# Kernel optimization log

Measured on AMD Instinct MI355X. Metric: run time of the kernel, lower is better.

## Reference

```python
import jax, jax.numpy as jnp
import numpy as np

EMBED_DIM = 1024
NUM_HEADS = 16
HEAD_DIM = EMBED_DIM // NUM_HEADS


def setup_inputs() -> dict:
    key = jax.random.key(0)
    kq, kk, kv, kw1, kw2 = jax.random.split(key, 5)
    B, S, D = 4, 2048, EMBED_DIM
    # xavier_uniform with gain=0.1
    lim_qkv = 0.1 * np.sqrt(6.0 / (D + 3 * D))
    lim_out = 0.1 * np.sqrt(6.0 / (D + D))
    return {
        "query": jax.random.normal(kq, (B, S, D), dtype=jnp.float32),
        "key": jax.random.normal(kk, (B, S, D), dtype=jnp.float32),
        "value": jax.random.normal(kv, (B, S, D), dtype=jnp.float32),
        "W_qkv": jax.random.uniform(kw1, (3 * D, D), jnp.float32, -lim_qkv, lim_qkv),
        "b_qkv": jnp.zeros((3 * D,), jnp.float32),
        "W_out": jax.random.uniform(kw2, (D, D), jnp.float32, -lim_out, lim_out),
        "b_out": jnp.zeros((D,), jnp.float32),
    }


def reference(query, key, value, W_qkv, b_qkv, W_out, b_out):
    # NOTE: the torch module computes Q,K,V all from `query` (self-attention);
    # `key`/`value` args are API placeholders and unused in the math.
    B, S, D = query.shape
    qkv = query @ W_qkv.T + b_qkv                     # [B,S,3D]
    qkv = qkv.reshape(B, S, 3, NUM_HEADS, HEAD_DIM)
    q = qkv[:, :, 0].transpose(0, 2, 1, 3)            # [B,H,S,hd]
    k = qkv[:, :, 1].transpose(0, 2, 1, 3)
    v = qkv[:, :, 2].transpose(0, 2, 1, 3)
    scale = 1.0 / np.sqrt(HEAD_DIM)
    scores = jnp.einsum("bhqd,bhkd->bhqk", q, k) * scale
    attn = jax.nn.softmax(scores, axis=-1)
    out = jnp.einsum("bhqk,bhkd->bhqd", attn, v)      # [B,H,S,hd]
    out = out.transpose(0, 2, 1, 3).reshape(B, S, D)
    return out @ W_out.T + b_out
```

## Files before the change

### kernel.cpp

```cpp
#include <hip/hip_runtime.h>

typedef __attribute__((ext_vector_type(8))) __bf16 bf16x8;
typedef __attribute__((ext_vector_type(4))) float f32x4;
typedef unsigned short u16;
typedef unsigned int u32;

__device__ __forceinline__ u16 f2bf(float x) {
  u32 u = __builtin_bit_cast(u32, x);
  u = (u + 0x7FFFu + ((u >> 16) & 1u)) >> 16;
  return (u16)u;
}

#define BAR()                          \
  {                                    \
    asm volatile("" ::: "memory");     \
    __builtin_amdgcn_s_barrier();      \
    asm volatile("" ::: "memory");     \
  }

__global__ __launch_bounds__(256) void cvt_f32_bf16(
    const float* __restrict__ in, u16* __restrict__ out, int n8) {
  int i = blockIdx.x * 256 + threadIdx.x;
  if (i >= n8) return;
  const float4* p = reinterpret_cast<const float4*>(in) + (size_t)i * 2;
  float4 a = p[0], b = p[1];
  uint4 r;
  r.x = (u32)f2bf(a.x) | ((u32)f2bf(a.y) << 16);
  r.y = (u32)f2bf(a.z) | ((u32)f2bf(a.w) << 16);
  r.z = (u32)f2bf(b.x) | ((u32)f2bf(b.y) << 16);
  r.w = (u32)f2bf(b.z) | ((u32)f2bf(b.w) << 16);
  reinterpret_cast<uint4*>(out)[i] = r;
}

__global__ __launch_bounds__(512, 2) void gemm_qkv8(
    const u16* __restrict__ A, const u16* __restrict__ Bw,
    const float* __restrict__ bias, u16* __restrict__ Qh,
    u16* __restrict__ Kh, u16* __restrict__ Vt) {
  constexpr int K = 1024;
  constexpr int NT = 16;
  __shared__ u16 Als[2][2][128][64];
  __shared__ u16 Bls[2][2][128][64];
  u16* const ALp = &Als[0][0][0][0];
  u16* const BLp = &Bls[0][0][0][0];

  const int tid = threadIdx.x;
  const int w = tid >> 6, l = tid & 63;
  const int kg = l >> 4, lr = l & 15;
  const int wr = w >> 2, wc = w & 3;
  const int bid = blockIdx.x;
  const int wg = (bid & 7) * 48 + (bid >> 3);
  const int tm = wg / 12, tn = wg % 12;

  const int r0 = tid >> 3, c0 = tid & 7;
  const int lc0 = c0 ^ (r0 & 7);
  const int ldsOff0 = tid * 8, ldsOff1 = tid * 8 + 4096;
  const u16* aSrc0[2];
  const u16* bSrc0[2];
#pragma unroll
  for (int h = 0; h < 2; ++h) {
    aSrc0[h] = A + (size_t)(tm * 256 + h * 128 + r0) * K + lc0 * 8;
    bSrc0[h] = Bw + (size_t)(tn * 256 + h * 128 + r0) * K + lc0 * 8;
  }
  const size_t rowStep = (size_t)64 * K;

#define ISSUE_A(BUF, H, T)                                                      \
  {                                                                             \
    __builtin_amdgcn_global_load_lds(                                           \
        (const __attribute__((address_space(1))) void*)(aSrc0[H] + (T) * 64),   \
        (__attribute__((address_space(3))) void*)(ALp + (BUF) * 16384 +         \
                                                 (H) * 8192 + ldsOff0),         \
        16, 0, 0);                                                              \
    __builtin_amdgcn_global_load_lds(                                           \
        (const __attribute__((address_space(1))) void*)(aSrc0[H] + rowStep +    \
                                                        (T) * 64),              \
        (__attribute__((address_space(3))) void*)(ALp + (BUF) * 16384 +         \
                                                 (H) * 8192 + ldsOff1),         \
        16, 0, 0);                                                              \
  }
#define ISSUE_B(BUF, H, T)                                                      \
  {                                                                             \
    __builtin_amdgcn_global_load_lds(                                           \
        (const __attribute__((address_space(1))) void*)(bSrc0[H] + (T) * 64),   \
        (__attribute__((address_space(3))) void*)(BLp + (BUF) * 16384 +         \
                                                 (H) * 8192 + ldsOff0),         \
        16, 0, 0);                                                              \
    __builtin_amdgcn_global_load_lds(                                           \
        (const __attribute__((address_space(1))) void*)(bSrc0[H] + rowStep +    \
                                                        (T) * 64),              \
        (__attribute__((address_space(3))) void*)(BLp + (BUF) * 16384 +         \
                                                 (H) * 8192 + ldsOff1),         \
        16, 0, 0);                                                              \
  }

  const int x7 = lr & 7;
  const int pc0 = (kg ^ x7) * 8;
  const int pc1 = ((kg + 4) ^ x7) * 8;
  const int wr16lr = wr * 16 + lr;
  const int wc16lr = wc * 16 + lr;

  const f32x4 fz = {0.f, 0.f, 0.f, 0.f};
  f32x4 acc[8][4];
#pragma unroll
  for (int m = 0; m < 8; ++m)
#pragma unroll
    for (int n = 0; n < 4; ++n) acc[m][n] = fz;

  bf16x8 aF[4][2], bF[2][2];

#define READ_A(P, MH)                                                           \
  {                                                                             \
    const u16* bp = ALp + (P) * 16384 + (MH) * 8192;                            \
    _Pragma("unroll") for (int mi = 0; mi < 4; ++mi) {                          \
      const u16* rp = bp + (mi * 32 + wr16lr) * 64;                             \
      aF[mi][0] = *(const bf16x8*)(rp + pc0);                                   \
      aF[mi][1] = *(const bf16x8*)(rp + pc1);                                   \
    }                                                                           \
  }
#define READ_B(P, NH)                                                           \
  {                                                                             \
    const u16* bp = BLp + (P) * 16384 + (NH) * 8192;                            \
    _Pragma("unroll") for (int ni = 0; ni < 2; ++ni) {                          \
      const u16* rp = bp + (ni * 64 + wc16lr) * 64;                             \
      bF[ni][0] = *(const bf16x8*)(rp + pc0);                                   \
      bF[ni][1] = *(const bf16x8*)(rp + pc1);                                   \
    }                                                                           \
  }
#define MFMA_Q(MH, NH)                                                          \
  {                                                                             \
    _Pragma("unroll") for (int mi = 0; mi < 4; ++mi)                            \
        _Pragma("unroll") for (int ni = 0; ni < 2; ++ni) {                      \
      acc[(MH)*4 + mi][(NH)*2 + ni] = __builtin_amdgcn_mfma_f32_16x16x32_bf16(  \
          aF[mi][0], bF[ni][0], acc[(MH)*4 + mi][(NH)*2 + ni], 0, 0, 0);        \
      acc[(MH)*4 + mi][(NH)*2 + ni] = __builtin_amdgcn_mfma_f32_16x16x32_bf16(  \
          aF[mi][1], bF[ni][1], acc[(MH)*4 + mi][(NH)*2 + ni], 0, 0, 0);        \
    }                                                                           \
  }

  ISSUE_A(0, 0, 0);
  ISSUE_A(0, 1, 0);
  ISSUE_B(0, 0, 0);
  ISSUE_B(0, 1, 0);
  ISSUE_A(1, 0, 1);
  ISSUE_B(1, 1, 1);

  for (int t = 0; t < NT; ++t) {
    const int p = t & 1;
    if (t == NT - 1) {
      asm volatile("s_waitcnt vmcnt(0)" ::: "memory");
    } else {
      asm volatile("s_waitcnt vmcnt(4)" ::: "memory");
    }
    BAR();
    if (t + 1 < NT) ISSUE_B(p ^ 1, 0, t + 1);
    READ_A(p, 0);
    READ_B(p, 0);
    BAR();
    __builtin_amdgcn_s_setprio(1);
    MFMA_Q(0, 0);
    __builtin_amdgcn_s_setprio(0);
    BAR();
    if (t + 1 < NT) ISSUE_A(p ^ 1, 1, t + 1);
    READ_B(p, 1);
    BAR();
    __builtin_amdgcn_s_setprio(1);
    MFMA_Q(0, 1);
    __builtin_amdgcn_s_setprio(0);
    BAR();
    if (t + 2 < NT) ISSUE_A(p, 0, t + 2);
    READ_A(p, 1);
    BAR();
    __builtin_amdgcn_s_setprio(1);
    MFMA_Q(1, 1);
    __builtin_amdgcn_s_setprio(0);
    BAR();
    if (t + 2 < NT) ISSUE_B(p, 1, t + 2);
    READ_B(p, 0);
    BAR();
    __builtin_amdgcn_s_setprio(1);
    MFMA_Q(1, 0);
    __builtin_amdgcn_s_setprio(0);
    BAR();
  }

#pragma unroll
  for (int m = 0; m < 8; ++m) {
    const int i0 = tm * 256 + m * 32 + wr * 16 + kg * 4;
    const int b = i0 >> 11, s0 = i0 & 2047;
#pragma unroll
    for (int n = 0; n < 4; ++n) {
      const int jc = tn * 256 + n * 64 + wc * 16 + lr;
      const float bs = bias[jc];
      const int sel = jc >> 10, hh = (jc >> 6) & 15, d = jc & 63;
      if (sel == 0) {
        u16* qp = Qh + ((size_t)((b * 16 + hh) * 2048 + s0)) * 64 + d;
#pragma unroll
        for (int j = 0; j < 4; ++j)
          qp[(size_t)j * 64] = f2bf((acc[m][n][j] + bs) * 0.18033688f);
      } else if (sel == 1) {
        u16* kp = Kh + ((size_t)((b * 16 + hh) * 2048 + s0)) * 64 + d;
#pragma unroll
        for (int j = 0; j < 4; ++j) kp[(size_t)j * 64] = f2bf(acc[m][n][j] + bs);
      } else {
        ushort4 vv;
        vv.x = f2bf(acc[m][n][0] + bs);
        vv.y = f2bf(acc[m][n][1] + bs);
        vv.z = f2bf(acc[m][n][2] + bs);
        vv.w = f2bf(acc[m][n][3] + bs);
        *(ushort4*)(Vt + ((size_t)((b * 16 + hh) * 64 + d)) * 2048 + s0) = vv;
      }
    }
  }
#undef ISSUE_A
#undef ISSUE_B
#undef READ_A
#undef READ_B
#undef MFMA_Q
}

__global__ __launch_bounds__(256) void gemm_out_k(
    const u16* __restrict__ A, const u16* __restrict__ Bw,
    const float* __restrict__ bias, float* __restrict__ Cout) {
  constexpr int N = 1024, K = 1024;
  __shared__ u16 As[128 * 32];
  __shared__ u16 Bs[128 * 32];
  const int tid = threadIdx.x;
  const int w = tid >> 6, l = tid & 63;
  const int kg = l >> 4, lr = l & 15;
  const int bid = blockIdx.x;
  const int wg = (bid & 7) * 64 + (bid >> 3);
  const int tm = wg >> 3, tn = wg & 7;
  const int wr = w >> 1, wc = w & 1;

  const u16* Ab = A + (size_t)tm * 128 * K;
  const u16* Bb = Bw + (size_t)tn * 128 * K;

  const f32x4 fz = {0.f, 0.f, 0.f, 0.f};
  f32x4 acc[4][4];
#pragma unroll
  for (int m = 0; m < 4; ++m)
#pragma unroll
    for (int n = 0; n < 4; ++n) acc[m][n] = fz;

  for (int k0 = 0; k0 < K; k0 += 32) {
#pragma unroll
    for (int u = 0; u < 2; ++u) {
      int e = u * 256 + tid;
      const u16* ga = Ab + (size_t)(e >> 2) * K + k0 + (e & 3) * 8;
      const u16* gb = Bb + (size_t)(e >> 2) * K + k0 + (e & 3) * 8;
      __builtin_amdgcn_global_load_lds(
          (const __attribute__((address_space(1))) void*)ga,
          (__attribute__((address_space(3))) void*)(As + (u * 256 + w * 64) * 8),
          16, 0, 0);
      __builtin_amdgcn_global_load_lds(
          (const __attribute__((address_space(1))) void*)gb,
          (__attribute__((address_space(3))) void*)(Bs + (u * 256 + w * 64) * 8),
          16, 0, 0);
    }
    asm volatile("s_waitcnt vmcnt(0)" ::: "memory");
    __syncthreads();
    bf16x8 a[4], b[4];
#pragma unroll
    for (int m = 0; m < 4; ++m)
      a[m] = *(const bf16x8*)(As + (wr * 64 + m * 16 + lr) * 32 + kg * 8);
#pragma unroll
    for (int n = 0; n < 4; ++n)
      b[n] = *(const bf16x8*)(Bs + (wc * 64 + n * 16 + lr) * 32 + kg * 8);
#pragma unroll
    for (int m = 0; m < 4; ++m)
#pragma unroll
      for (int n = 0; n < 4; ++n)
        acc[m][n] =
            __builtin_amdgcn_mfma_f32_16x16x32_bf16(a[m], b[n], acc[m][n], 0, 0, 0);
    __syncthreads();
  }

#pragma unroll
  for (int m = 0; m < 4; ++m) {
    const int i0 = tm * 128 + wr * 64 + m * 16 + kg * 4;
#pragma unroll
    for (int n = 0; n < 4; ++n) {
      const int jc = tn * 128 + wc * 64 + n * 16 + lr;
      const float bs = bias[jc];
#pragma unroll
      for (int j = 0; j < 4; ++j)
        Cout[(size_t)(i0 + j) * N + jc] = acc[m][n][j] + bs;
    }
  }
}

__global__ __launch_bounds__(256, 4) void attn_kernel(
    const u16* __restrict__ Qh, const u16* __restrict__ Kh,
    const u16* __restrict__ Vt, u16* __restrict__ Aout) {
  __shared__ alignas(16) u16 Kl[2][4096];
  __shared__ alignas(16) u16 Vl[2][4096];
  const int tid = threadIdx.x;
  const int w = tid >> 6, l = tid & 63;
  const int kg = l >> 4, lq = l & 15;
  const int bid = blockIdx.x;
  const int wgi = (bid & 7) * 128 + (bid >> 3);
  const int bh = wgi >> 4, qt = wgi & 15;
  const int qbase = qt * 128 + w * 32;

  const u16* Qb = Qh + ((size_t)(bh * 2048 + qbase + lq)) * 64;
  const bf16x8 aq00 = *(const bf16x8*)(Qb + kg * 8);
  const bf16x8 aq01 = *(const bf16x8*)(Qb + 32 + kg * 8);
  const bf16x8 aq10 = *(const bf16x8*)(Qb + 16 * 64 + kg * 8);
  const bf16x8 aq11 = *(const bf16x8*)(Qb + 16 * 64 + 32 + kg * 8);

  const u16* Kb = Kh + (size_t)bh * 2048 * 64;
  const u16* Vb = Vt + (size_t)bh * 64 * 2048;

  const int r7K = 4 * (lq >> 3) + (lq & 3);
  const int rowbK = 8 * ((lq >> 2) & 1) + r7K;
  const int ckK0 = (kg ^ r7K) * 8;
  const int ckK1 = ((kg + 4) ^ r7K) * 8;
  const int r7V = lq & 7;
  const int ckV0 = (kg ^ r7V) * 8;
  const int ckV1 = ((kg + 4) ^ r7V) * 8;

  const f32x4 fz = {0.f, 0.f, 0.f, 0.f};
  f32x4 on0[4] = {fz, fz, fz, fz};
  f32x4 on1[4] = {fz, fz, fz, fz};
  float m0 = -1e30f, m1 = -1e30f, l0 = 0.f, l1 = 0.f;

#define STAGE_KV(buf, kc)                                                        \
  {                                                                              \
    {                                                                            \
      const int s_ = tid, row_ = s_ >> 3, c_ = s_ & 7;                           \
      const int sw_ = (c_ ^ (row_ & 7)) * 8;                                     \
      const int srow_ = (row_ & ~20) | ((row_ & 4) << 2) | ((row_ & 16) >> 2);   \
      __builtin_amdgcn_global_load_lds(                                          \
          (const __attribute__((address_space(1))) void*)(Kb + (size_t)((kc) + srow_) * 64 + sw_), \
          (__attribute__((address_space(3))) void*)(&Kl[buf][s_ * 8]), 16, 0, 0);\
      __builtin_amdgcn_global_load_lds(                                          \
          (const __attribute__((address_space(1))) void*)(Vb + (size_t)row_ * 2048 + (kc) + sw_),  \
          (__attribute__((address_space(3))) void*)(&Vl[buf][s_ * 8]), 16, 0, 0);\
    }                                                                            \
    {                                                                            \
      const int s_ = 256 + tid, row_ = s_ >> 3, c_ = s_ & 7;                     \
      const int sw_ = (c_ ^ (row_ & 7)) * 8;                                     \
      const int srow_ = (row_ & ~20) | ((row_ & 4) << 2) | ((row_ & 16) >> 2);   \
      __builtin_amdgcn_global_load_lds(                                          \
          (const __attribute__((address_space(1))) void*)(Kb + (size_t)((kc) + srow_) * 64 + sw_), \
          (__attribute__((address_space(3))) void*)(&Kl[buf][s_ * 8]), 16, 0, 0);\
      __builtin_amdgcn_global_load_lds(                                          \
          (const __attribute__((address_space(1))) void*)(Vb + (size_t)row_ * 2048 + (kc) + sw_),  \
          (__attribute__((address_space(3))) void*)(&Vl[buf][s_ * 8]), 16, 0, 0);\
    }                                                                            \
  }

  STAGE_KV(0, 0);
  asm volatile("s_waitcnt vmcnt(0)" ::: "memory");
  __syncthreads();

  int cur = 0;
  for (int kc = 0; kc < 2048; kc += 64) {
    if (kc + 64 < 2048) STAGE_KV(cur ^ 1, kc + 64);
    const u16* Klc = Kl[cur];
    const u16* Vlc = Vl[cur];

    f32x4 st0[4], st1[4];
    __builtin_amdgcn_s_setprio(1);
#pragma unroll
    for (int t = 0; t < 4; ++t) {
      const int ro = (rowbK + ((t >> 1) * 32 + (t & 1) * 16)) * 64;
      bf16x8 k0 = *(const bf16x8*)(Klc + ro + ckK0);
      bf16x8 k1 = *(const bf16x8*)(Klc + ro + ckK1);
      f32x4 z0 = fz, z1 = fz;
      z0 = __builtin_amdgcn_mfma_f32_16x16x32_bf16(k0, aq00, z0, 0, 0, 0);
      z0 = __builtin_amdgcn_mfma_f32_16x16x32_bf16(k1, aq01, z0, 0, 0, 0);
      z1 = __builtin_amdgcn_mfma_f32_16x16x32_bf16(k0, aq10, z1, 0, 0, 0);
      z1 = __builtin_amdgcn_mfma_f32_16x16x32_bf16(k1, aq11, z1, 0, 0, 0);
      st0[t] = z0;
      st1[t] = z1;
    }
    __builtin_amdgcn_s_setprio(0);

    float rm0 = st0[0][0], rm1 = st1[0][0];
#pragma unroll
    for (int t = 0; t < 4; ++t)
#pragma unroll
      for (int j = 0; j < 4; ++j) {
        rm0 = fmaxf(rm0, st0[t][j]);
        rm1 = fmaxf(rm1, st1[t][j]);
      }
    rm0 = fmaxf(rm0, __shfl_xor(rm0, 16));
    rm0 = fmaxf(rm0, __shfl_xor(rm0, 32));
    rm1 = fmaxf(rm1, __shfl_xor(rm1, 16));
    rm1 = fmaxf(rm1, __shfl_xor(rm1, 32));
    if (!__all(fmaxf(rm0 - m0, rm1 - m1) <= 8.f)) {
      float mn0 = fmaxf(m0, rm0), mn1 = fmaxf(m1, rm1);
      float a0 = __builtin_amdgcn_exp2f(m0 - mn0);
      float a1 = __builtin_amdgcn_exp2f(m1 - mn1);
      m0 = mn0;
      m1 = mn1;
      l0 *= a0;
      l1 *= a1;
#pragma unroll
      for (int j = 0; j < 4; ++j) {
        float aj0 = __shfl(a0, kg * 4 + j);
        float aj1 = __shfl(a1, kg * 4 + j);
#pragma unroll
        for (int n = 0; n < 4; ++n) {
          on0[n][j] *= aj0;
          on1[n][j] *= aj1;
        }
      }
    }

    bf16x8 pa00, pa01, pa10, pa11;
    {
      float rs = 0.f;
      float p[4][4];
#pragma unroll
      for (int t = 0; t < 4; ++t)
#pragma unroll
        for (int j = 0; j < 4; ++j) {
          p[t][j] = __builtin_amdgcn_exp2f(st0[t][j] - m0);
          rs += p[t][j];
        }
      rs += __shfl_xor(rs, 16);
      rs += __shfl_xor(rs, 32);
      l0 += rs;
#pragma unroll
      for (int j = 0; j < 4; ++j) {
        pa00[j] = (__bf16)p[0][j];
        pa00[4 + j] = (__bf16)p[1][j];
        pa01[j] = (__bf16)p[2][j];
        pa01[4 + j] = (__bf16)p[3][j];
      }
    }
    {
      float rs = 0.f;
      float p[4][4];
#pragma unroll
      for (int t = 0; t < 4; ++t)
#pragma unroll
        for (int j = 0; j < 4; ++j) {
          p[t][j] = __builtin_amdgcn_exp2f(st1[t][j] - m1);
          rs += p[t][j];
        }
      rs += __shfl_xor(rs, 16);
      rs += __shfl_xor(rs, 32);
      l1 += rs;
#pragma unroll
      for (int j = 0; j < 4; ++j) {
        pa10[j] = (__bf16)p[0][j];
        pa10[4 + j] = (__bf16)p[1][j];
        pa11[j] = (__bf16)p[2][j];
        pa11[4 + j] = (__bf16)p[3][j];
      }
    }

    __builtin_amdgcn_s_setprio(1);
#pragma unroll
    for (int n = 0; n < 4; ++n) {
      const int ro = (n * 16 + lq) * 64;
      bf16x8 v0 = *(const bf16x8*)(Vlc + ro + ckV0);
      bf16x8 v1 = *(const bf16x8*)(Vlc + ro + ckV1);
      on0[n] = __builtin_amdgcn_mfma_f32_16x16x32_bf16(pa00, v0, on0[n], 0, 0, 0);
      on0[n] = __builtin_amdgcn_mfma_f32_16x16x32_bf16(pa01, v1, on0[n], 0, 0, 0);
      on1[n] = __builtin_amdgcn_mfma_f32_16x16x32_bf16(pa10, v0, on1[n], 0, 0, 0);
      on1[n] = __builtin_amdgcn_mfma_f32_16x16x32_bf16(pa11, v1, on1[n], 0, 0, 0);
    }
    __builtin_amdgcn_s_setprio(0);

    asm volatile("s_waitcnt vmcnt(0)" ::: "memory");
    __syncthreads();
    cur ^= 1;
  }

  const int b = bh >> 4, h = bh & 15;
  {
    u16* Ob = Aout + (size_t)(b * 2048 + qbase + kg * 4) * 1024 + h * 64 + lq;
#pragma unroll
    for (int j = 0; j < 4; ++j) {
      float lj = __shfl(l0, kg * 4 + j);
      float inv = 1.f / lj;
#pragma unroll
      for (int n = 0; n < 4; ++n)
        Ob[(size_t)j * 1024 + n * 16] = f2bf(on0[n][j] * inv);
    }
  }
  {
    u16* Ob = Aout + (size_t)(b * 2048 + qbase + 16 + kg * 4) * 1024 + h * 64 + lq;
#pragma unroll
    for (int j = 0; j < 4; ++j) {
      float lj = __shfl(l1, kg * 4 + j);
      float inv = 1.f / lj;
#pragma unroll
      for (int n = 0; n < 4; ++n)
        Ob[(size_t)j * 1024 + n * 16] = f2bf(on1[n][j] * inv);
    }
  }
}

extern "C" void kernel_launch(void* const* d_in, const int* in_sizes, int n_in,
                              void* d_out, int out_size, void* d_ws, size_t ws_size,
                              hipStream_t stream) {
  const float* query = (const float*)d_in[0];
  const float* Wqkv = (const float*)d_in[3];
  const float* bqkv = (const float*)d_in[4];
  const float* Wout = (const float*)d_in[5];
  const float* bout = (const float*)d_in[6];
  float* out = (float*)d_out;

  char* ws = (char*)d_ws;
  u16* qx = (u16*)(ws);
  u16* wqkvb = (u16*)(ws + 16777216);
  u16* woutb = (u16*)(ws + 23068672);
  u16* Qh = (u16*)(ws + 25165824);
  u16* Kh = (u16*)(ws + 41943040);
  u16* Vt = (u16*)(ws + 58720256);
  u16* attn = qx;

  cvt_f32_bf16<<<4096, 256, 0, stream>>>(query, qx, 8388608 / 8);
  cvt_f32_bf16<<<1536, 256, 0, stream>>>(Wqkv, wqkvb, 3145728 / 8);
  cvt_f32_bf16<<<512, 256, 0, stream>>>(Wout, woutb, 1048576 / 8);

  gemm_qkv8<<<384, 512, 0, stream>>>(qx, wqkvb, bqkv, Qh, Kh, Vt);
  attn_kernel<<<1024, 256, 0, stream>>>(Qh, Kh, Vt, attn);
  gemm_out_k<<<512, 256, 0, stream>>>(attn, woutb, bout, out);
}
```

Before: 211.4 us.

## Merge conversion launches and compute softmax row sums via MFMA with ones

Fuses the three f32-to-bf16 conversion kernels into one launch that picks its source by thread index, removing two kernel launches. In the attention loop, the per-row sum of probabilities is now taken with extra MFMA ops against a vector of ones, which replaces the VALU adds and cross-lane shuffles. The row max reduction is rewritten as chained max pairs, which may allow three-operand max instructions. The MFMA row sum is accumulated from bf16-rounded probabilities, so it slightly changes numerics, and it adds four MFMAs per tile.

```diff
diff --git a/kernel.cpp b/kernel.cpp
--- a/kernel.cpp
+++ b/kernel.cpp
@@ -18,18 +18,29 @@
     asm volatile("" ::: "memory");     \
   }
 
-__global__ __launch_bounds__(256) void cvt_f32_bf16(
-    const float* __restrict__ in, u16* __restrict__ out, int n8) {
+__global__ __launch_bounds__(256) void cvt3(
+    const float* __restrict__ q, const float* __restrict__ w1,
+    const float* __restrict__ w2, u16* __restrict__ oq, u16* __restrict__ ow1,
+    u16* __restrict__ ow2) {
   int i = blockIdx.x * 256 + threadIdx.x;
-  if (i >= n8) return;
-  const float4* p = reinterpret_cast<const float4*>(in) + (size_t)i * 2;
+  const float* in;
+  u16* out;
+  int base;
+  if (i < 1048576) {
+    in = q; out = oq; base = i;
+  } else if (i < 1441792) {
+    in = w1; out = ow1; base = i - 1048576;
+  } else {
+    in = w2; out = ow2; base = i - 1441792;
+  }
+  const float4* p = reinterpret_cast<const float4*>(in) + (size_t)base * 2;
   float4 a = p[0], b = p[1];
   uint4 r;
   r.x = (u32)f2bf(a.x) | ((u32)f2bf(a.y) << 16);
   r.y = (u32)f2bf(a.z) | ((u32)f2bf(a.w) << 16);
   r.z = (u32)f2bf(b.x) | ((u32)f2bf(b.y) << 16);
   r.w = (u32)f2bf(b.z) | ((u32)f2bf(b.w) << 16);
-  reinterpret_cast<uint4*>(out)[i] = r;
+  reinterpret_cast<uint4*>(out)[base] = r;
 }
 
 __global__ __launch_bounds__(512, 2) void gemm_qkv8(
@@ -318,10 +329,15 @@
   const int ckV0 = (kg ^ r7V) * 8;
   const int ckV1 = ((kg + 4) ^ r7V) * 8;
 
+  bf16x8 vone;
+#pragma unroll
+  for (int i = 0; i < 8; ++i) vone[i] = (__bf16)1.0f;
+
   const f32x4 fz = {0.f, 0.f, 0.f, 0.f};
   f32x4 on0[4] = {fz, fz, fz, fz};
   f32x4 on1[4] = {fz, fz, fz, fz};
-  float m0 = -1e30f, m1 = -1e30f, l0 = 0.f, l1 = 0.f;
+  f32x4 ls0 = fz, ls1 = fz;
+  float m0 = -1e30f, m1 = -1e30f;
 
 #define STAGE_KV(buf, kc)                                                        \
   {                                                                              \
@@ -376,14 +392,23 @@
     }
     __builtin_amdgcn_s_setprio(0);
 
-    float rm0 = st0[0][0], rm1 = st1[0][0];
-#pragma unroll
-    for (int t = 0; t < 4; ++t)
-#pragma unroll
-      for (int j = 0; j < 4; ++j) {
-        rm0 = fmaxf(rm0, st0[t][j]);
-        rm1 = fmaxf(rm1, st1[t][j]);
-      }
+    float rm0, rm1;
+    rm0 = fmaxf(fmaxf(st0[0][0], st0[0][1]), st0[0][2]);
+    rm0 = fmaxf(fmaxf(rm0, st0[0][3]), st0[1][0]);
+    rm0 = fmaxf(fmaxf(rm0, st0[1][1]), st0[1][2]);
+    rm0 = fmaxf(fmaxf(rm0, st0[1][3]), st0[2][0]);
+    rm0 = fmaxf(fmaxf(rm0, st0[2][1]), st0[2][2]);
+    rm0 = fmaxf(fmaxf(rm0, st0[2][3]), st0[3][0]);
+    rm0 = fmaxf(fmaxf(rm0, st0[3][1]), st0[3][2]);
+    rm0 = fmaxf(rm0, st0[3][3]);
+    rm1 = fmaxf(fmaxf(st1[0][0], st1[0][1]), st1[0][2]);
+    rm1 = fmaxf(fmaxf(rm1, st1[0][3]), st1[1][0]);
+    rm1 = fmaxf(fmaxf(rm1, st1[1][1]), st1[1][2]);
+    rm1 = fmaxf(fmaxf(rm1, st1[1][3]), st1[2][0]);
+    rm1 = fmaxf(fmaxf(rm1, st1[2][1]), st1[2][2]);
+    rm1 = fmaxf(fmaxf(rm1, st1[2][3]), st1[3][0]);
+    rm1 = fmaxf(fmaxf(rm1, st1[3][1]), st1[3][2]);
+    rm1 = fmaxf(rm1, st1[3][3]);
     rm0 = fmaxf(rm0, __shfl_xor(rm0, 16));
     rm0 = fmaxf(rm0, __shfl_xor(rm0, 32));
     rm1 = fmaxf(rm1, __shfl_xor(rm1, 16));
@@ -394,12 +419,12 @@
       float a1 = __builtin_amdgcn_exp2f(m1 - mn1);
       m0 = mn0;
       m1 = mn1;
-      l0 *= a0;
-      l1 *= a1;
 #pragma unroll
       for (int j = 0; j < 4; ++j) {
         float aj0 = __shfl(a0, kg * 4 + j);
         float aj1 = __shfl(a1, kg * 4 + j);
+        ls0[j] *= aj0;
+        ls1[j] *= aj1;
 #pragma unroll
         for (int n = 0; n < 4; ++n) {
           on0[n][j] *= aj0;
@@ -409,50 +434,23 @@
     }
 
     bf16x8 pa00, pa01, pa10, pa11;
-    {
-      float rs = 0.f;
-      float p[4][4];
-#pragma unroll
-      for (int t = 0; t < 4; ++t)
-#pragma unroll
-        for (int j = 0; j < 4; ++j) {
-          p[t][j] = __builtin_amdgcn_exp2f(st0[t][j] - m0);
-          rs += p[t][j];
-        }
-      rs += __shfl_xor(rs, 16);
-      rs += __shfl_xor(rs, 32);
-      l0 += rs;
-#pragma unroll
-      for (int j = 0; j < 4; ++j) {
-        pa00[j] = (__bf16)p[0][j];
-        pa00[4 + j] = (__bf16)p[1][j];
-        pa01[j] = (__bf16)p[2][j];
-        pa01[4 + j] = (__bf16)p[3][j];
-      }
-    }
-    {
-      float rs = 0.f;
-      float p[4][4];
-#pragma unroll
-      for (int t = 0; t < 4; ++t)
-#pragma unroll
-        for (int j = 0; j < 4; ++j) {
-          p[t][j] = __builtin_amdgcn_exp2f(st1[t][j] - m1);
-          rs += p[t][j];
-        }
-      rs += __shfl_xor(rs, 16);
-      rs += __shfl_xor(rs, 32);
-      l1 += rs;
-#pragma unroll
-      for (int j = 0; j < 4; ++j) {
-        pa10[j] = (__bf16)p[0][j];
-        pa10[4 + j] = (__bf16)p[1][j];
-        pa11[j] = (__bf16)p[2][j];
-        pa11[4 + j] = (__bf16)p[3][j];
-      }
+#pragma unroll
+    for (int j = 0; j < 4; ++j) {
+      pa00[j] = (__bf16)__builtin_amdgcn_exp2f(st0[0][j] - m0);
+      pa00[4 + j] = (__bf16)__builtin_amdgcn_exp2f(st0[1][j] - m0);
+      pa01[j] = (__bf16)__builtin_amdgcn_exp2f(st0[2][j] - m0);
+      pa01[4 + j] = (__bf16)__builtin_amdgcn_exp2f(st0[3][j] - m0);
+      pa10[j] = (__bf16)__builtin_amdgcn_exp2f(st1[0][j] - m1);
+      pa10[4 + j] = (__bf16)__builtin_amdgcn_exp2f(st1[1][j] - m1);
+      pa11[j] = (__bf16)__builtin_amdgcn_exp2f(st1[2][j] - m1);
+      pa11[4 + j] = (__bf16)__builtin_amdgcn_exp2f(st1[3][j] - m1);
     }
 
     __builtin_amdgcn_s_setprio(1);
+    ls0 = __builtin_amdgcn_mfma_f32_16x16x32_bf16(pa00, vone, ls0, 0, 0, 0);
+    ls0 = __builtin_amdgcn_mfma_f32_16x16x32_bf16(pa01, vone, ls0, 0, 0, 0);
+    ls1 = __builtin_amdgcn_mfma_f32_16x16x32_bf16(pa10, vone, ls1, 0, 0, 0);
+    ls1 = __builtin_amdgcn_mfma_f32_16x16x32_bf16(pa11, vone, ls1, 0, 0, 0);
 #pragma unroll
     for (int n = 0; n < 4; ++n) {
       const int ro = (n * 16 + lq) * 64;
@@ -475,8 +473,7 @@
     u16* Ob = Aout + (size_t)(b * 2048 + qbase + kg * 4) * 1024 + h * 64 + lq;
 #pragma unroll
     for (int j = 0; j < 4; ++j) {
-      float lj = __shfl(l0, kg * 4 + j);
-      float inv = 1.f / lj;
+      float inv = 1.f / ls0[j];
 #pragma unroll
       for (int n = 0; n < 4; ++n)
         Ob[(size_t)j * 1024 + n * 16] = f2bf(on0[n][j] * inv);
@@ -486,8 +483,7 @@
     u16* Ob = Aout + (size_t)(b * 2048 + qbase + 16 + kg * 4) * 1024 + h * 64 + lq;
 #pragma unroll
     for (int j = 0; j < 4; ++j) {
-      float lj = __shfl(l1, kg * 4 + j);
-      float inv = 1.f / lj;
+      float inv = 1.f / ls1[j];
 #pragma unroll
       for (int n = 0; n < 4; ++n)
         Ob[(size_t)j * 1024 + n * 16] = f2bf(on1[n][j] * inv);
@@ -514,9 +510,7 @@
   u16* Vt = (u16*)(ws + 58720256);
   u16* attn = qx;
 
-  cvt_f32_bf16<<<4096, 256, 0, stream>>>(query, qx, 8388608 / 8);
-  cvt_f32_bf16<<<1536, 256, 0, stream>>>(Wqkv, wqkvb, 3145728 / 8);
-  cvt_f32_bf16<<<512, 256, 0, stream>>>(Wout, woutb, 1048576 / 8);
+  cvt3<<<6144, 256, 0, stream>>>(query, Wqkv, Wout, qx, wqkvb, woutb);
 
   gemm_qkv8<<<384, 512, 0, stream>>>(qx, wqkvb, bqkv, Qh, Kh, Vt);
   attn_kernel<<<1024, 256, 0, stream>>>(Qh, Kh, Vt, attn);
```

Result: faster. 201.4 us (-4.7%).
